# Kernel optimization log

Hardware: AMD Instinct MI355X
Metric: run time of the kernel (lower is better)

## Reference

```python
import jax, jax.numpy as jnp
import numpy as np


def setup_inputs() -> dict:
    key = jax.random.key(0)
    k1, k2, k3, k4 = jax.random.split(key, 4)
    B, N, D, L = 4, 512, 256, 64
    x = jax.random.normal(k1, (B, N, D), dtype=jnp.float32)
    adj = jax.random.uniform(k2, (B, N, N), dtype=jnp.float32)
    W_proj = jax.random.normal(k3, (L, D), dtype=jnp.float32) * (1.0 / np.sqrt(D))
    learn_w = jax.random.uniform(k4, (L,), dtype=jnp.float32)  # init.uniform_(0,1)
    return {"x": x, "adj": adj, "W_proj": W_proj, "learn_w": learn_w}


def reference(x, adj, W_proj, learn_w):
    # x: [B,N,D]; projection (no bias): x_hat [B,N,L]
    x_hat = jnp.einsum('bnd,ld->bnl', x, W_proj)
    # pairwise L1-style abs difference: [B,N,N,L]
    diff = jnp.abs(x_hat[:, :, None, :] - x_hat[:, None, :, :])
    # weighted reduce over feature dim: [B,N,N]
    dist = jnp.einsum('bijl,l->bij', diff, learn_w)
    out = jax.nn.leaky_relu(dist, negative_slope=0.01)
    out = out - jnp.max(out, axis=-1, keepdims=True)
    soft_adj = adj * jnp.exp(out)
    # NOTE: faithful to original: epsilon added AFTER the division
    soft_adj = soft_adj / jnp.sum(soft_adj, axis=-1, keepdims=True) + 1e-10
    return soft_adj
```

## Files before the change

kernel.cpp:

```cpp
#include <hip/hip_runtime.h>
#include <hip/hip_bf16.h>
#include <math.h>

#define BB 4
#define NN 512
#define DD 256
#define LL 64

#define K1_NR 4
#define IPB  4
#define WSTRIDE 132

__global__ __launch_bounds__(256) void k1_proj(const float* __restrict__ x,
                                               const float* __restrict__ Wp,
                                               float* __restrict__ xhatT) {
  __shared__ __align__(16) float Wl[LL * WSTRIDE];
  __shared__ __align__(16) float xs[K1_NR * DD];
  const int bx = blockIdx.x;
  const int b  = bx / (NN / K1_NR);
  const int n0 = (bx % (NN / K1_NR)) * K1_NR;
  const int t  = threadIdx.x;
  const int l  = t & 63;
  const int r  = t >> 6;

  #pragma unroll
  for (int k = 0; k < K1_NR; ++k)
    xs[k * DD + t] = x[((size_t)(b * NN + n0 + k)) * DD + t];

  float4 acc4 = make_float4(0.f, 0.f, 0.f, 0.f);
  #pragma unroll
  for (int h = 0; h < 2; ++h) {
    __syncthreads();
    #pragma unroll
    for (int kk = 0; kk < 32; ++kk) {
      int idx = kk * 256 + t;
      int ll  = idx >> 7;
      int dd  = idx & 127;
      Wl[ll * WSTRIDE + dd] = Wp[ll * DD + h * 128 + dd];
    }
    __syncthreads();
    const float4* xrow = (const float4*)&xs[r * DD + h * 128];
    const float4* wrow = (const float4*)&Wl[l * WSTRIDE];
    #pragma unroll 4
    for (int dd = 0; dd < 32; ++dd) {
      float4 xv = xrow[dd];
      float4 wv = wrow[dd];
      acc4.x += xv.x * wv.x;
      acc4.y += xv.y * wv.y;
      acc4.z += xv.z * wv.z;
      acc4.w += xv.w * wv.w;
    }
  }
  float acc = (acc4.x + acc4.y) + (acc4.z + acc4.w);
  xhatT[(size_t)b * (LL * NN) + (size_t)l * NN + (n0 + r)] = acc;
}

__global__ __launch_bounds__(512) void k2_main(const float* __restrict__ xhatT,
                                               const float* __restrict__ adj,
                                               const float* __restrict__ lw,
                                               float* __restrict__ out) {
  __shared__ __align__(16) float xi_s[LL * IPB];
  __shared__ float w_s[LL];
  __shared__ float redm[IPB * 8];
  __shared__ float reds[IPB * 8];

  const int bx   = blockIdx.x;
  const int b    = bx / (NN / IPB);
  const int i0   = (bx % (NN / IPB)) * IPB;
  const int t    = threadIdx.x;
  const int wave = t >> 6;
  const int lane = t & 63;

  const float* xb = xhatT + (size_t)b * (LL * NN);

  if (t < LL * IPB) {
    int l = t >> 2, r = t & 3;
    xi_s[t] = lw[l] * xb[l * NN + i0 + r];
  }
  if (t < LL) w_s[t] = lw[t];
  __syncthreads();

  float acc[IPB];
  #pragma unroll
  for (int r = 0; r < IPB; ++r) acc[r] = 0.f;

  const float4* xi4 = (const float4*)xi_s;
  #pragma unroll 4
  for (int l = 0; l < LL; ++l) {
    float pj = w_s[l] * xb[l * NN + t];
    float4 a = xi4[l];
    acc[0] += fabsf(a.x - pj);
    acc[1] += fabsf(a.y - pj);
    acc[2] += fabsf(a.z - pj);
    acc[3] += fabsf(a.w - pj);
  }

  #pragma unroll
  for (int r = 0; r < IPB; ++r) {
    float d = acc[r];
    acc[r] = d >= 0.f ? d : 0.01f * d;
  }

  #pragma unroll
  for (int r = 0; r < IPB; ++r) {
    float m = acc[r];
    #pragma unroll
    for (int off = 32; off > 0; off >>= 1)
      m = fmaxf(m, __shfl_xor(m, off, 64));
    if (lane == 0) redm[r * 8 + wave] = m;
  }
  __syncthreads();

  float e[IPB];
  const float* adjb = adj + ((size_t)b * NN + i0) * NN;
  #pragma unroll
  for (int r = 0; r < IPB; ++r) {
    float m = redm[r * 8 + 0];
    #pragma unroll
    for (int k = 1; k < 8; ++k) m = fmaxf(m, redm[r * 8 + k]);
    e[r] = adjb[(size_t)r * NN + t] * __expf(acc[r] - m);
  }

  #pragma unroll
  for (int r = 0; r < IPB; ++r) {
    float s = e[r];
    #pragma unroll
    for (int off = 32; off > 0; off >>= 1)
      s += __shfl_xor(s, off, 64);
    if (lane == 0) reds[r * 8 + wave] = s;
  }
  __syncthreads();

  float* outb = out + ((size_t)b * NN + i0) * NN;
  #pragma unroll
  for (int r = 0; r < IPB; ++r) {
    float s = reds[r * 8 + 0];
    #pragma unroll
    for (int k = 1; k < 8; ++k) s += reds[r * 8 + k];
    outb[(size_t)r * NN + t] = e[r] / s + 1e-10f;
  }
}

extern "C" void kernel_launch(void* const* d_in, const int* in_sizes, int n_in,
                              void* d_out, int out_size, void* d_ws, size_t ws_size,
                              hipStream_t stream) {
  const float* x   = (const float*)d_in[0];
  const float* adj = (const float*)d_in[1];
  const float* Wp  = (const float*)d_in[2];
  const float* lw  = (const float*)d_in[3];
  float* out   = (float*)d_out;
  float* xhatT = (float*)d_ws;

  hipLaunchKernelGGL(k1_proj, dim3(BB * NN / K1_NR), dim3(256), 0, stream,
                     x, Wp, xhatT);
  hipLaunchKernelGGL(k2_main, dim3(BB * NN / IPB), dim3(512), 0, stream,
                     xhatT, adj, lw, out);
}
```

Before: 76.51 us.

## Fold learn_w into projection and prefetch xhat and adj in registers

The projection kernel now scales each W_proj row by learn_w, which is valid because learn_w is nonnegative (uniform 0..1), so |w·a - w·b| = w·|a-b|. It also loads the full W tile in one pass using float4 loads, with a wider padded stride, and drops the two-half loop and its extra syncs. The main kernel preloads all 64 xhat_j values and the adj row values into registers before the barrier, so global latency overlaps the shared-memory setup. It adds a launch_bounds occupancy hint and removes the per-iteration learn_w multiply, at the cost of higher register pressure from the 64-element register array.

```diff
diff --git a/kernel.cpp b/kernel.cpp
--- a/kernel.cpp
+++ b/kernel.cpp
@@ -1,5 +1,4 @@
 #include <hip/hip_runtime.h>
-#include <hip/hip_bf16.h>
 #include <math.h>
 
 #define BB 4
@@ -8,91 +7,93 @@
 #define LL 64
 
 #define K1_NR 4
+#define WST  260
 #define IPB  4
-#define WSTRIDE 132
 
 __global__ __launch_bounds__(256) void k1_proj(const float* __restrict__ x,
                                                const float* __restrict__ Wp,
+                                               const float* __restrict__ lw,
                                                float* __restrict__ xhatT) {
-  __shared__ __align__(16) float Wl[LL * WSTRIDE];
+  __shared__ __align__(16) float Wl[LL * WST];
   __shared__ __align__(16) float xs[K1_NR * DD];
   const int bx = blockIdx.x;
-  const int b  = bx / (NN / K1_NR);
-  const int n0 = (bx % (NN / K1_NR)) * K1_NR;
+  const int b  = bx >> 7;
+  const int n0 = (bx & 127) * K1_NR;
   const int t  = threadIdx.x;
   const int l  = t & 63;
   const int r  = t >> 6;
 
+  const float4* Wp4 = (const float4*)Wp;
   #pragma unroll
-  for (int k = 0; k < K1_NR; ++k)
-    xs[k * DD + t] = x[((size_t)(b * NN + n0 + k)) * DD + t];
+  for (int it = 0; it < 16; ++it) {
+    int idx = it * 256 + t;
+    int ll  = idx >> 6;
+    int dq  = idx & 63;
+    float4 wv = Wp4[idx];
+    float  w  = lw[ll];
+    wv.x *= w; wv.y *= w; wv.z *= w; wv.w *= w;
+    *(float4*)&Wl[ll * WST + dq * 4] = wv;
+  }
+  ((float4*)xs)[t] = ((const float4*)x)[((size_t)(b * NN + n0)) * (DD / 4) + t];
+  __syncthreads();
 
-  float4 acc4 = make_float4(0.f, 0.f, 0.f, 0.f);
-  #pragma unroll
-  for (int h = 0; h < 2; ++h) {
-    __syncthreads();
-    #pragma unroll
-    for (int kk = 0; kk < 32; ++kk) {
-      int idx = kk * 256 + t;
-      int ll  = idx >> 7;
-      int dd  = idx & 127;
-      Wl[ll * WSTRIDE + dd] = Wp[ll * DD + h * 128 + dd];
-    }
-    __syncthreads();
-    const float4* xrow = (const float4*)&xs[r * DD + h * 128];
-    const float4* wrow = (const float4*)&Wl[l * WSTRIDE];
-    #pragma unroll 4
-    for (int dd = 0; dd < 32; ++dd) {
-      float4 xv = xrow[dd];
-      float4 wv = wrow[dd];
-      acc4.x += xv.x * wv.x;
-      acc4.y += xv.y * wv.y;
-      acc4.z += xv.z * wv.z;
-      acc4.w += xv.w * wv.w;
-    }
+  const float4* xrow = (const float4*)&xs[r * DD];
+  const float4* wrow = (const float4*)&Wl[l * WST];
+  float4 a = make_float4(0.f, 0.f, 0.f, 0.f);
+  #pragma unroll 8
+  for (int dd = 0; dd < 64; ++dd) {
+    float4 xv = xrow[dd];
+    float4 wv = wrow[dd];
+    a.x += xv.x * wv.x;
+    a.y += xv.y * wv.y;
+    a.z += xv.z * wv.z;
+    a.w += xv.w * wv.w;
   }
-  float acc = (acc4.x + acc4.y) + (acc4.z + acc4.w);
-  xhatT[(size_t)b * (LL * NN) + (size_t)l * NN + (n0 + r)] = acc;
+  xhatT[(size_t)b * (LL * NN) + (size_t)l * NN + (n0 + r)] = (a.x + a.y) + (a.z + a.w);
 }
 
-__global__ __launch_bounds__(512) void k2_main(const float* __restrict__ xhatT,
-                                               const float* __restrict__ adj,
-                                               const float* __restrict__ lw,
-                                               float* __restrict__ out) {
+__global__ __launch_bounds__(512, 4) void k2_main(const float* __restrict__ xhatT,
+                                                  const float* __restrict__ adj,
+                                                  float* __restrict__ out) {
   __shared__ __align__(16) float xi_s[LL * IPB];
-  __shared__ float w_s[LL];
   __shared__ float redm[IPB * 8];
   __shared__ float reds[IPB * 8];
 
   const int bx   = blockIdx.x;
-  const int b    = bx / (NN / IPB);
-  const int i0   = (bx % (NN / IPB)) * IPB;
+  const int b    = bx >> 7;
+  const int i0   = (bx & 127) * IPB;
   const int t    = threadIdx.x;
   const int wave = t >> 6;
   const int lane = t & 63;
 
   const float* xb = xhatT + (size_t)b * (LL * NN);
 
+  float xj[LL];
+  #pragma unroll
+  for (int l = 0; l < LL; ++l) xj[l] = xb[l * NN + t];
+
+  const float* adjb = adj + ((size_t)b * NN + i0) * NN;
+  float adjv[IPB];
+  #pragma unroll
+  for (int r = 0; r < IPB; ++r) adjv[r] = adjb[(size_t)r * NN + t];
+
   if (t < LL * IPB) {
-    int l = t >> 2, r = t & 3;
-    xi_s[t] = lw[l] * xb[l * NN + i0 + r];
+    int l = t >> 2, rr = t & 3;
+    xi_s[t] = xb[l * NN + i0 + rr];
   }
-  if (t < LL) w_s[t] = lw[t];
   __syncthreads();
 
-  float acc[IPB];
+  float acc[IPB] = {0.f, 0.f, 0.f, 0.f};
+  const float4* xi4 = (const float4*)xi_s;
   #pragma unroll
-  for (int r = 0; r < IPB; ++r) acc[r] = 0.f;
-
-  const float4* xi4 = (const float4*)xi_s;
-  #pragma unroll 4
   for (int l = 0; l < LL; ++l) {
-    float pj = w_s[l] * xb[l * NN + t];
     float4 a = xi4[l];
-    acc[0] += fabsf(a.x - pj);
-    acc[1] += fabsf(a.y - pj);
-    acc[2] += fabsf(a.z - pj);
-    acc[3] += fabsf(a.w - pj);
+    float  p = xj[l];
+    acc[0] += fabsf(a.x - p);
+    acc[1] += fabsf(a.y - p);
+    acc[2] += fabsf(a.z - p);
+    acc[3] += fabsf(a.w - p);
+    if ((l & 7) == 7) asm volatile("" ::: "memory");
   }
 
   #pragma unroll
@@ -112,13 +113,12 @@
   __syncthreads();
 
   float e[IPB];
-  const float* adjb = adj + ((size_t)b * NN + i0) * NN;
   #pragma unroll
   for (int r = 0; r < IPB; ++r) {
     float m = redm[r * 8 + 0];
     #pragma unroll
     for (int k = 1; k < 8; ++k) m = fmaxf(m, redm[r * 8 + k]);
-    e[r] = adjb[(size_t)r * NN + t] * __expf(acc[r] - m);
+    e[r] = adjv[r] * __expf(acc[r] - m);
   }
 
   #pragma unroll
@@ -152,7 +152,7 @@
   float* xhatT = (float*)d_ws;
 
   hipLaunchKernelGGL(k1_proj, dim3(BB * NN / K1_NR), dim3(256), 0, stream,
-                     x, Wp, xhatT);
+                     x, Wp, lw, xhatT);
   hipLaunchKernelGGL(k2_main, dim3(BB * NN / IPB), dim3(512), 0, stream,
-                     xhatT, adj, lw, out);
+                     xhatT, adj, out);
 }
```

Result: slower. 231.0 us (+201.9%).
